# Kernel optimization log

Hardware: AMD Instinct MI355X
Metric: run time of the kernel (lower is better)

## Reference

```python
import jax, jax.numpy as jnp
import numpy as np

B, S, H, DFF, E, K = 2, 2048, 1024, 2048, 8, 2


def setup_inputs() -> dict:
    key = jax.random.key(0)
    ks = jax.random.split(key, 8)
    sc_h = 1.0 / np.sqrt(H)
    sc_f = 1.0 / np.sqrt(DFF)
    x = jax.random.normal(ks[0], (B, S, H), dtype=jnp.float32)
    Wg = jax.random.uniform(ks[1], (E, H), jnp.float32, -sc_h, sc_h)  # gate (no bias)
    W1 = jax.random.uniform(ks[2], (E, DFF, H), jnp.float32, -sc_h, sc_h)  # SiGLU gate proj
    b1 = jax.random.uniform(ks[3], (E, DFF), jnp.float32, -sc_h, sc_h)
    W2 = jax.random.uniform(ks[4], (E, DFF, H), jnp.float32, -sc_h, sc_h)  # SiGLU value proj
    b2 = jax.random.uniform(ks[5], (E, DFF), jnp.float32, -sc_h, sc_h)
    W3 = jax.random.uniform(ks[6], (E, H, DFF), jnp.float32, -sc_f, sc_f)  # down proj
    b3 = jax.random.uniform(ks[7], (E, H), jnp.float32, -sc_f, sc_f)
    return {"x": x, "Wg": Wg, "W1": W1, "b1": b1, "W2": W2, "b2": b2, "W3": W3, "b3": b3}


def _moe(x, Wg, W1, b1, W2, b2, W3, b3):
    Bm, Sm, Hm = x.shape
    xt = x.reshape(-1, Hm)  # [T, H]
    gout = xt @ Wg.T  # [T, E]
    topv, topi = jax.lax.top_k(gout, K)  # [T, K]
    w = jax.nn.softmax(topv, axis=-1)  # [T, K]
    # combine weights per expert: comb[t, e] = sum_k w[t,k] * 1[topi[t,k]==e]
    comb = jnp.einsum('tke,tk->te', jax.nn.one_hot(topi, E, dtype=x.dtype), w)  # [T, E]
    # dense per-expert FFN (fixed-shape equivalent of the gather/scatter loop)
    g = jnp.einsum('th,efh->etf', xt, W1) + b1[:, None, :]  # [E, T, DFF]
    v = jnp.einsum('th,efh->etf', xt, W2) + b2[:, None, :]
    h = jax.nn.silu(g) * v  # SiGLU
    eo = jnp.einsum('etf,ehf->eth', h, W3) + b3[:, None, :]  # [E, T, H]
    out = jnp.einsum('eth,te->th', eo, comb)
    return out.reshape(Bm, Sm, Hm)


def reference(x, Wg, W1, b1, W2, b2, W3, b3):
    return _moe(x, Wg, W1, b1, W2, b2, W3, b3)
```

## Files before the change

### kernel.cpp

```cpp
#include <hip/hip_runtime.h>
#include <hip/hip_bf16.h>

#define T_TOK 4096
#define H_DIM 1024
#define DFF_D 2048
#define E_NUM 8
#define K_TOP 2
#define MAXJOBS64 136
#define MAXJOBS128 72
#define CVT_BLOCKS 2048
#define EO_OFF ((size_t)T_TOK * K_TOP * H_DIM)

typedef __attribute__((ext_vector_type(8))) short s16x8;
typedef __attribute__((ext_vector_type(4))) float f32x4;

__device__ __forceinline__ ushort f2bf(float f) {
    unsigned u = __float_as_uint(f);
    u = (u + 0x7FFFu + ((u >> 16) & 1u)) >> 16;
    return (ushort)u;
}

__device__ __forceinline__ float bf2f(short s) {
    return __uint_as_float(((unsigned)(ushort)s) << 16);
}

__device__ __forceinline__ void glds16(const ushort* g, ushort* l) {
    __builtin_amdgcn_global_load_lds(
        (const __attribute__((address_space(1))) unsigned*)g,
        (__attribute__((address_space(3))) unsigned*)l, 16, 0, 0);
}

__device__ __forceinline__ s16x8 lds_frag(const ushort* base, int row, int bytecol) {
    int byte = row * 128 + (bytecol ^ ((row & 7) << 4));
    return *(const s16x8*)((const char*)base + byte);
}

__device__ __forceinline__ void cvt8(const float* p, ushort* dst, size_t i) {
    float4 a = ((const float4*)(p + i * 8))[0];
    float4 b = ((const float4*)(p + i * 8))[1];
    union { ushort us[8]; uint4 q; } o;
    o.us[0] = f2bf(a.x); o.us[1] = f2bf(a.y); o.us[2] = f2bf(a.z); o.us[3] = f2bf(a.w);
    o.us[4] = f2bf(b.x); o.us[5] = f2bf(b.y); o.us[6] = f2bf(b.z); o.us[7] = f2bf(b.w);
    ((uint4*)dst)[i] = o.q;
}

__global__ __launch_bounds__(256) void cvt_kernel(
    const float* __restrict__ in, ushort* __restrict__ out, int n8)
{
    int i = blockIdx.x * blockDim.x + threadIdx.x;
    const int stride = gridDim.x * blockDim.x;
    for (; i < n8; i += stride) cvt8(in, out, i);
}

__global__ __launch_bounds__(256) void cvtW_gate_kernel(
    const float* __restrict__ W1, ushort* __restrict__ w1bf,
    const float* __restrict__ W2, ushort* __restrict__ w2bf,
    const float* __restrict__ W3, ushort* __restrict__ w3bf,
    const float* __restrict__ x,  const float* __restrict__ Wg,
    int* __restrict__ topi_packed, float* __restrict__ wt_slot,
    ushort* __restrict__ xbf)
{
    if ((int)blockIdx.x < CVT_BLOCKS) {
        const int nW = E_NUM * DFF_D * H_DIM / 8;
        const int total = (W3 != nullptr) ? 3 * nW : 2 * nW;
        int i = blockIdx.x * 256 + threadIdx.x;
        const int stride = CVT_BLOCKS * 256;
        for (; i < total; i += stride) {
            if (i < nW)            cvt8(W1, w1bf, i);
            else if (i < 2 * nW)   cvt8(W2, w2bf, i - nW);
            else                   cvt8(W3, w3bf, i - 2 * nW);
        }
        return;
    }
    const int t = (blockIdx.x - CVT_BLOCKS) * 4 + (threadIdx.x >> 6);
    const int lane = threadIdx.x & 63;
    const float* xr = x + (size_t)t * H_DIM;
    float xv[16];
    #pragma unroll
    for (int j = 0; j < 16; ++j) xv[j] = xr[j * 64 + lane];

    ushort* xo = xbf + (size_t)t * H_DIM;
    #pragma unroll
    for (int j = 0; j < 16; ++j) xo[j * 64 + lane] = f2bf(xv[j]);

    float score[E_NUM];
    #pragma unroll
    for (int e = 0; e < E_NUM; ++e) {
        const float* wr = Wg + e * H_DIM;
        float p = 0.f;
        #pragma unroll
        for (int j = 0; j < 16; ++j) p += xv[j] * wr[j * 64 + lane];
        #pragma unroll
        for (int s = 32; s >= 1; s >>= 1) p += __shfl_xor(p, s, 64);
        score[e] = p;
    }
    if (lane == 0) {
        int i0 = 0;
        #pragma unroll
        for (int e = 1; e < E_NUM; ++e) if (score[e] > score[i0]) i0 = e;
        int i1 = (i0 == 0) ? 1 : 0;
        #pragma unroll
        for (int e = 0; e < E_NUM; ++e)
            if (e != i0 && score[e] > score[i1]) i1 = e;
        float e1 = expf(score[i1] - score[i0]);
        float w0 = 1.f / (1.f + e1);
        float w1 = e1 / (1.f + e1);
        topi_packed[t] = i0 | (i1 << 8);
        wt_slot[t * K_TOP + 0] = w0;
        wt_slot[t * K_TOP + 1] = w1;
    }
}

__global__ __launch_bounds__(256) void build_lists(
    const int* __restrict__ topi_packed,
    int* __restrict__ cnt, int* __restrict__ tok_list, int* __restrict__ slot_list)
{
    const int e = blockIdx.x;
    __shared__ int lcnt;
    if (threadIdx.x == 0) lcnt = 0;
    __syncthreads();
    for (int t = threadIdx.x; t < T_TOK; t += 256) {
        int pk = topi_packed[t];
        int i0 = pk & 0xff;
        int i1 = (pk >> 8) & 0xff;
        if (i0 == e) {
            int p = atomicAdd(&lcnt, 1);
            tok_list[e * T_TOK + p] = t;
            slot_list[e * T_TOK + p] = t * K_TOP + 0;
        }
        if (i1 == e) {
            int p = atomicAdd(&lcnt, 1);
            tok_list[e * T_TOK + p] = t;
            slot_list[e * T_TOK + p] = t * K_TOP + 1;
        }
    }
    __syncthreads();
    if (threadIdx.x == 0) cnt[e] = lcnt;
}

__global__ void build_jobs(const int* __restrict__ cnt,
                           int* __restrict__ jobs64, int* __restrict__ jobs128,
                           int* __restrict__ njobs)
{
    if (threadIdx.x == 0 && blockIdx.x == 0) {
        int n = 0, n2 = 0;
        for (int e = 0; e < E_NUM; ++e) {
            int mt = (cnt[e] + 63) >> 6;
            for (int m = 0; m < mt; ++m) jobs64[n++] = (e << 16) | m;
            int mt2 = (cnt[e] + 127) >> 7;
            for (int m = 0; m < mt2; ++m) jobs128[n2++] = (e << 16) | m;
        }
        njobs[0] = n;
        njobs[1] = n2;
    }
}

__global__ __launch_bounds__(256) void up_kernel(
    const ushort* __restrict__ xbf,
    const ushort* __restrict__ w1bf, const float* __restrict__ b1,
    const ushort* __restrict__ w2bf, const float* __restrict__ b2,
    const int* __restrict__ cnt, const int* __restrict__ tok_list,
    const int* __restrict__ slot_list, const float* __restrict__ wt_slot,
    const int* __restrict__ jobs128, const int* __restrict__ njobs,
    ushort* __restrict__ h)
{
    if ((int)blockIdx.y >= njobs[1]) return;
    const int jb = jobs128[blockIdx.y];
    const int e = jb >> 16;
    const int mbase = (jb & 0xffff) * 128;
    const int M = cnt[e];
    const int nbase = blockIdx.x * 64;
    const int tid = threadIdx.x;
    const int lane = tid & 63;
    const int w = tid >> 6;

    __shared__ ushort As[128 * 64];
    __shared__ ushort B1s[64 * 64];
    __shared__ ushort B2s[64 * 64];

    const ushort* srcA[4];
    const ushort* srcB1[2];
    const ushort* srcB2[2];
    #pragma unroll
    for (int j = 0; j < 4; ++j) {
        int o = j * 4096 + tid * 16;
        int r = o >> 7;
        int cb = (o & 127) ^ ((r & 7) << 4);
        int lpos = mbase + r; if (lpos > M - 1) lpos = M - 1;
        int tok = tok_list[e * T_TOK + lpos];
        srcA[j] = xbf + (size_t)tok * H_DIM + (cb >> 1);
    }
    #pragma unroll
    for (int j = 0; j < 2; ++j) {
        int o = j * 4096 + tid * 16;
        int r = o >> 7;
        int cb = (o & 127) ^ ((r & 7) << 4);
        srcB1[j] = w1bf + ((size_t)e * DFF_D + nbase + r) * H_DIM + (cb >> 1);
        srcB2[j] = w2bf + ((size_t)e * DFF_D + nbase + r) * H_DIM + (cb >> 1);
    }

    const f32x4 zero = {0.f, 0.f, 0.f, 0.f};
    f32x4 accg[2][4], accv[2][4];
    #pragma unroll
    for (int mi = 0; mi < 2; ++mi)
        #pragma unroll
        for (int ni = 0; ni < 4; ++ni) { accg[mi][ni] = zero; accv[mi][ni] = zero; }

    const int r16 = lane & 15;
    const int g4  = lane >> 4;
    const int cb0 = g4 * 16;

    for (int k0 = 0; k0 < H_DIM; k0 += 64) {
        #pragma unroll
        for (int j = 0; j < 4; ++j)
            glds16(srcA[j] + k0, &As[j * 2048 + tid * 8]);
        #pragma unroll
        for (int j = 0; j < 2; ++j) {
            glds16(srcB1[j] + k0, &B1s[j * 2048 + tid * 8]);
            glds16(srcB2[j] + k0, &B2s[j * 2048 + tid * 8]);
        }
        __syncthreads();
        #pragma unroll
        for (int kk = 0; kk < 2; ++kk) {
            s16x8 bf1[4], bf2[4];
            #pragma unroll
            for (int ni = 0; ni < 4; ++ni) {
                bf1[ni] = lds_frag(B1s, ni * 16 + r16, kk * 64 + cb0);
                bf2[ni] = lds_frag(B2s, ni * 16 + r16, kk * 64 + cb0);
            }
            #pragma unroll
            for (int mi = 0; mi < 2; ++mi) {
                s16x8 af = lds_frag(As, w * 32 + mi * 16 + r16, kk * 64 + cb0);
                #pragma unroll
                for (int ni = 0; ni < 4; ++ni) {
                    accg[mi][ni] = __builtin_amdgcn_mfma_f32_16x16x32_bf16(af, bf1[ni], accg[mi][ni], 0, 0, 0);
                    accv[mi][ni] = __builtin_amdgcn_mfma_f32_16x16x32_bf16(af, bf2[ni], accv[mi][ni], 0, 0, 0);
                }
            }
        }
        __syncthreads();
    }

    #pragma unroll
    for (int mi = 0; mi < 2; ++mi) {
        #pragma unroll
        for (int j = 0; j < 4; ++j) {
            int p = mbase + w * 32 + mi * 16 + g4 * 4 + j;
            if (p < M) {
                int slot = slot_list[e * T_TOK + p];
                float wgt = wt_slot[slot];
                #pragma unroll
                for (int ni = 0; ni < 4; ++ni) {
                    int col = nbase + ni * 16 + r16;
                    float g = accg[mi][ni][j] + b1[e * DFF_D + col];
                    float v = accv[mi][ni][j] + b2[e * DFF_D + col];
                    float s = g / (1.f + __expf(-g));
                    h[(size_t)slot * DFF_D + col] = f2bf(wgt * s * v);
                }
            }
        }
    }
}

__global__ __launch_bounds__(128) void down_kernel(
    const ushort* __restrict__ h,
    const ushort* __restrict__ w3bf,
    const int* __restrict__ cnt, const int* __restrict__ slot_list,
    const int* __restrict__ jobs128, const int* __restrict__ njobs,
    ushort* __restrict__ eo)
{
    if ((int)blockIdx.y >= njobs[1]) return;
    const int jb = jobs128[blockIdx.y];
    const int e = jb >> 16;
    const int mbase = (jb & 0xffff) * 128;
    const int M = cnt[e];
    const int nbase = (blockIdx.x >> 1) * 64;
    const int kc = blockIdx.x & 1;
    const int kbeg = kc * (DFF_D / 2);
    const int tid = threadIdx.x;
    const int lane = tid & 63;
    const int w = tid >> 6;

    __shared__ ushort As[128 * 64];
    __shared__ ushort Bs[64 * 64];

    const ushort* srcA[8];
    #pragma unroll
    for (int j = 0; j < 8; ++j) {
        int o = j * 2048 + tid * 16;
        int r = o >> 7;
        int cb = (o & 127) ^ ((r & 7) << 4);
        int lpos = mbase + r; if (lpos > M - 1) lpos = M - 1;
        int slot = slot_list[e * T_TOK + lpos];
        srcA[j] = h + (size_t)slot * DFF_D + kbeg + (cb >> 1);
    }
    const ushort* srcB[4];
    #pragma unroll
    for (int j = 0; j < 4; ++j) {
        int o = j * 2048 + tid * 16;
        int r = o >> 7;
        int cb = (o & 127) ^ ((r & 7) << 4);
        srcB[j] = w3bf + ((size_t)e * H_DIM + nbase + r) * DFF_D + kbeg + (cb >> 1);
    }

    const f32x4 zero = {0.f, 0.f, 0.f, 0.f};
    f32x4 acc[4][4];
    #pragma unroll
    for (int mi = 0; mi < 4; ++mi)
        #pragma unroll
        for (int ni = 0; ni < 4; ++ni) acc[mi][ni] = zero;

    const int r16 = lane & 15;
    const int g4  = lane >> 4;
    const int cb0 = g4 * 16;

    for (int k0 = 0; k0 < DFF_D / 2; k0 += 64) {
        #pragma unroll
        for (int j = 0; j < 8; ++j)
            glds16(srcA[j] + k0, &As[j * 1024 + tid * 8]);
        #pragma unroll
        for (int j = 0; j < 4; ++j)
            glds16(srcB[j] + k0, &Bs[j * 1024 + tid * 8]);
        __syncthreads();
        #pragma unroll
        for (int kk = 0; kk < 2; ++kk) {
            s16x8 bf[4];
            #pragma unroll
            for (int ni = 0; ni < 4; ++ni)
                bf[ni] = lds_frag(Bs, ni * 16 + r16, kk * 64 + cb0);
            #pragma unroll
            for (int mi = 0; mi < 4; ++mi) {
                s16x8 af = lds_frag(As, w * 64 + mi * 16 + r16, kk * 64 + cb0);
                #pragma unroll
                for (int ni = 0; ni < 4; ++ni)
                    acc[mi][ni] = __builtin_amdgcn_mfma_f32_16x16x32_bf16(af, bf[ni], acc[mi][ni], 0, 0, 0);
            }
        }
        __syncthreads();
    }

    ushort* eop = eo + (size_t)kc * EO_OFF;
    #pragma unroll
    for (int mi = 0; mi < 4; ++mi) {
        #pragma unroll
        for (int j = 0; j < 4; ++j) {
            int p = mbase + w * 64 + mi * 16 + g4 * 4 + j;
            if (p < M) {
                int slot = slot_list[e * T_TOK + p];
                #pragma unroll
                for (int ni = 0; ni < 4; ++ni) {
                    int col = nbase + ni * 16 + r16;
                    eop[(size_t)slot * H_DIM + col] = f2bf(acc[mi][ni][j]);
                }
            }
        }
    }
}

__global__ __launch_bounds__(256) void combine_kernel(
    const ushort* __restrict__ eo, const int* __restrict__ topi_packed,
    const float* __restrict__ wt_slot, const float* __restrict__ b3,
    float* __restrict__ out)
{
    const int i = blockIdx.x * 256 + threadIdx.x;
    const int t = i >> 7;
    const int c0 = (i & 127) * 8;
    const int pk = topi_packed[t];
    const int e0 = pk & 0xff, e1 = (pk >> 8) & 0xff;
    const float w0 = wt_slot[2 * t], w1 = wt_slot[2 * t + 1];
    s16x8 a0 = *(const s16x8*)(eo + (size_t)(2 * t) * H_DIM + c0);
    s16x8 b0 = *(const s16x8*)(eo + (size_t)(2 * t + 1) * H_DIM + c0);
    s16x8 a1 = *(const s16x8*)(eo + EO_OFF + (size_t)(2 * t) * H_DIM + c0);
    s16x8 b1 = *(const s16x8*)(eo + EO_OFF + (size_t)(2 * t + 1) * H_DIM + c0);
    const float4* p0 = (const float4*)(b3 + e0 * H_DIM + c0);
    const float4* p1 = (const float4*)(b3 + e1 * H_DIM + c0);
    float4 b0a = p0[0], b0b = p0[1];
    float4 b1a = p1[0], b1b = p1[1];
    float r[8];
    #pragma unroll
    for (int j = 0; j < 8; ++j)
        r[j] = (bf2f(a0[j]) + bf2f(a1[j])) + (bf2f(b0[j]) + bf2f(b1[j]));
    float4 r0, r1;
    r0.x = r[0] + w0 * b0a.x + w1 * b1a.x;
    r0.y = r[1] + w0 * b0a.y + w1 * b1a.y;
    r0.z = r[2] + w0 * b0a.z + w1 * b1a.z;
    r0.w = r[3] + w0 * b0a.w + w1 * b1a.w;
    r1.x = r[4] + w0 * b0b.x + w1 * b1b.x;
    r1.y = r[5] + w0 * b0b.y + w1 * b1b.y;
    r1.z = r[6] + w0 * b0b.z + w1 * b1b.z;
    r1.w = r[7] + w0 * b0b.w + w1 * b1b.w;
    float4* op = (float4*)(out + (size_t)t * H_DIM + c0);
    op[0] = r0;
    op[1] = r1;
}

extern "C" void kernel_launch(void* const* d_in, const int* in_sizes, int n_in,
                              void* d_out, int out_size, void* d_ws, size_t ws_size,
                              hipStream_t stream) {
    const float* x  = (const float*)d_in[0];
    const float* Wg = (const float*)d_in[1];
    const float* W1 = (const float*)d_in[2];
    const float* b1 = (const float*)d_in[3];
    const float* W2 = (const float*)d_in[4];
    const float* b2 = (const float*)d_in[5];
    const float* W3 = (const float*)d_in[6];
    const float* b3 = (const float*)d_in[7];
    float* out = (float*)d_out;

    char* ws = (char*)d_ws;
    int*   cnt       = (int*)(ws);
    int*   njobs     = (int*)(ws + 64);
    int*   jobs64    = (int*)(ws + 128);
    int*   jobs128   = (int*)(ws + 704);
    int*   tok_list  = (int*)(ws + 1024);
    int*   slot_list = (int*)(ws + 1024 + E_NUM * T_TOK * 4);
    float* wt_slot   = (float*)(ws + 1024 + 2 * E_NUM * T_TOK * 4);
    int*   topi      = (int*)(ws + 320 * 1024);
    ushort* xbf  = (ushort*)(ws + (size_t)1  * (1u << 20));
    ushort* w1bf = (ushort*)(ws + (size_t)16 * (1u << 20));
    ushort* w2bf = (ushort*)(ws + (size_t)48 * (1u << 20));
    ushort* hbuf = (ushort*)(ws + (size_t)80 * (1u << 20));
    ushort* eobf = (ushort*)(ws + (size_t)4  * (1u << 20));

    const bool bigws = ws_size >= ((size_t)147 << 20);
    ushort* w3bf = bigws ? (ushort*)(ws + (size_t)114 * (1u << 20))
                         : (ushort*)(ws + (size_t)40  * (1u << 20));

    cvtW_gate_kernel<<<CVT_BLOCKS + T_TOK / 4, 256, 0, stream>>>(
        W1, w1bf, W2, w2bf, bigws ? W3 : nullptr, w3bf,
        x, Wg, topi, wt_slot, xbf);

    build_lists<<<E_NUM, 256, 0, stream>>>(topi, cnt, tok_list, slot_list);
    build_jobs<<<1, 64, 0, stream>>>(cnt, jobs64, jobs128, njobs);

    dim3 gup(DFF_D / 64, MAXJOBS128);
    up_kernel<<<gup, 256, 0, stream>>>(xbf, w1bf, b1, w2bf, b2, cnt, tok_list,
                                       slot_list, wt_slot, jobs128, njobs, hbuf);

    if (!bigws)
        cvt_kernel<<<2048, 256, 0, stream>>>(W3, w3bf, E_NUM * H_DIM * DFF_D / 8);

    dim3 gdn((H_DIM / 64) * 2, MAXJOBS128);
    down_kernel<<<gdn, 128, 0, stream>>>(hbuf, w3bf, cnt, slot_list,
                                         jobs128, njobs, eobf);

    combine_kernel<<<T_TOK * H_DIM / 8 / 256, 256, 0, stream>>>(eobf, topi, wt_slot, b3, out);
}
```

Before: 257.2 us.

## Fold W3 conversion into up_kernel grid and derive jobs inline from counts

Removes the single-thread build_jobs launch; each GEMM block now derives its expert and row tile directly from cnt. In the big-workspace path, W3 fp32-to-bf16 conversion moves out of the first conversion kernel into extra block rows of up_kernel, so it overlaps with the up-projection GEMM instead of delaying gating. The eo buffers are split into two explicit pointers, which moves the second one to a new workspace offset. The risk is that the conversion blocks compete with the GEMM blocks for bandwidth and compute units.

```diff
diff --git a/kernel.cpp b/kernel.cpp
--- a/kernel.cpp
+++ b/kernel.cpp
@@ -6,10 +6,9 @@
 #define DFF_D 2048
 #define E_NUM 8
 #define K_TOP 2
-#define MAXJOBS64 136
 #define MAXJOBS128 72
 #define CVT_BLOCKS 2048
-#define EO_OFF ((size_t)T_TOK * K_TOP * H_DIM)
+#define W3_ROWS 8
 
 typedef __attribute__((ext_vector_type(8))) short s16x8;
 typedef __attribute__((ext_vector_type(4))) float f32x4;
@@ -44,6 +43,19 @@
     ((uint4*)dst)[i] = o.q;
 }
 
+__device__ __forceinline__ bool job_from_y(const int* cnt, int y, int& e, int& mbase, int& M) {
+    int n = 0; mbase = -1;
+    #pragma unroll
+    for (int ee = 0; ee < E_NUM; ++ee) {
+        int t = (cnt[ee] + 127) >> 7;
+        if (mbase < 0 && y < n + t) { e = ee; mbase = (y - n) * 128; }
+        n += t;
+    }
+    if (mbase < 0) return false;
+    M = cnt[e];
+    return true;
+}
+
 __global__ __launch_bounds__(256) void cvt_kernel(
     const float* __restrict__ in, ushort* __restrict__ out, int n8)
 {
@@ -55,20 +67,17 @@
 __global__ __launch_bounds__(256) void cvtW_gate_kernel(
     const float* __restrict__ W1, ushort* __restrict__ w1bf,
     const float* __restrict__ W2, ushort* __restrict__ w2bf,
-    const float* __restrict__ W3, ushort* __restrict__ w3bf,
     const float* __restrict__ x,  const float* __restrict__ Wg,
     int* __restrict__ topi_packed, float* __restrict__ wt_slot,
     ushort* __restrict__ xbf)
 {
     if ((int)blockIdx.x < CVT_BLOCKS) {
         const int nW = E_NUM * DFF_D * H_DIM / 8;
-        const int total = (W3 != nullptr) ? 3 * nW : 2 * nW;
         int i = blockIdx.x * 256 + threadIdx.x;
         const int stride = CVT_BLOCKS * 256;
-        for (; i < total; i += stride) {
-            if (i < nW)            cvt8(W1, w1bf, i);
-            else if (i < 2 * nW)   cvt8(W2, w2bf, i - nW);
-            else                   cvt8(W3, w3bf, i - 2 * nW);
+        for (; i < 2 * nW; i += stride) {
+            if (i < nW) cvt8(W1, w1bf, i);
+            else        cvt8(W2, w2bf, i - nW);
         }
         return;
     }
@@ -138,37 +147,26 @@
     if (threadIdx.x == 0) cnt[e] = lcnt;
 }
 
-__global__ void build_jobs(const int* __restrict__ cnt,
-                           int* __restrict__ jobs64, int* __restrict__ jobs128,
-                           int* __restrict__ njobs)
-{
-    if (threadIdx.x == 0 && blockIdx.x == 0) {
-        int n = 0, n2 = 0;
-        for (int e = 0; e < E_NUM; ++e) {
-            int mt = (cnt[e] + 63) >> 6;
-            for (int m = 0; m < mt; ++m) jobs64[n++] = (e << 16) | m;
-            int mt2 = (cnt[e] + 127) >> 7;
-            for (int m = 0; m < mt2; ++m) jobs128[n2++] = (e << 16) | m;
-        }
-        njobs[0] = n;
-        njobs[1] = n2;
-    }
-}
-
 __global__ __launch_bounds__(256) void up_kernel(
     const ushort* __restrict__ xbf,
     const ushort* __restrict__ w1bf, const float* __restrict__ b1,
     const ushort* __restrict__ w2bf, const float* __restrict__ b2,
     const int* __restrict__ cnt, const int* __restrict__ tok_list,
     const int* __restrict__ slot_list, const float* __restrict__ wt_slot,
-    const int* __restrict__ jobs128, const int* __restrict__ njobs,
+    const float* __restrict__ W3src, ushort* __restrict__ w3dst,
     ushort* __restrict__ h)
 {
-    if ((int)blockIdx.y >= njobs[1]) return;
-    const int jb = jobs128[blockIdx.y];
-    const int e = jb >> 16;
-    const int mbase = (jb & 0xffff) * 128;
-    const int M = cnt[e];
+    if ((int)blockIdx.y >= MAXJOBS128) {
+        if (W3src != nullptr) {
+            const int nW3 = E_NUM * H_DIM * DFF_D / 8;
+            int i = ((blockIdx.y - MAXJOBS128) * gridDim.x + blockIdx.x) * 256 + threadIdx.x;
+            const int stride = W3_ROWS * gridDim.x * 256;
+            for (; i < nW3; i += stride) cvt8(W3src, w3dst, i);
+        }
+        return;
+    }
+    int e, mbase, M;
+    if (!job_from_y(cnt, blockIdx.y, e, mbase, M)) return;
     const int nbase = blockIdx.x * 64;
     const int tid = threadIdx.x;
     const int lane = tid & 63;
@@ -266,14 +264,10 @@
     const ushort* __restrict__ h,
     const ushort* __restrict__ w3bf,
     const int* __restrict__ cnt, const int* __restrict__ slot_list,
-    const int* __restrict__ jobs128, const int* __restrict__ njobs,
-    ushort* __restrict__ eo)
-{
-    if ((int)blockIdx.y >= njobs[1]) return;
-    const int jb = jobs128[blockIdx.y];
-    const int e = jb >> 16;
-    const int mbase = (jb & 0xffff) * 128;
-    const int M = cnt[e];
+    ushort* __restrict__ eo0, ushort* __restrict__ eo1)
+{
+    int e, mbase, M;
+    if (!job_from_y(cnt, blockIdx.y, e, mbase, M)) return;
     const int nbase = (blockIdx.x >> 1) * 64;
     const int kc = blockIdx.x & 1;
     const int kbeg = kc * (DFF_D / 2);
@@ -339,7 +333,7 @@
         __syncthreads();
     }
 
-    ushort* eop = eo + (size_t)kc * EO_OFF;
+    ushort* eop = kc ? eo1 : eo0;
     #pragma unroll
     for (int mi = 0; mi < 4; ++mi) {
         #pragma unroll
@@ -358,7 +352,8 @@
 }
 
 __global__ __launch_bounds__(256) void combine_kernel(
-    const ushort* __restrict__ eo, const int* __restrict__ topi_packed,
+    const ushort* __restrict__ eo0, const ushort* __restrict__ eo1,
+    const int* __restrict__ topi_packed,
     const float* __restrict__ wt_slot, const float* __restrict__ b3,
     float* __restrict__ out)
 {
@@ -368,10 +363,10 @@
     const int pk = topi_packed[t];
     const int e0 = pk & 0xff, e1 = (pk >> 8) & 0xff;
     const float w0 = wt_slot[2 * t], w1 = wt_slot[2 * t + 1];
-    s16x8 a0 = *(const s16x8*)(eo + (size_t)(2 * t) * H_DIM + c0);
-    s16x8 b0 = *(const s16x8*)(eo + (size_t)(2 * t + 1) * H_DIM + c0);
-    s16x8 a1 = *(const s16x8*)(eo + EO_OFF + (size_t)(2 * t) * H_DIM + c0);
-    s16x8 b1 = *(const s16x8*)(eo + EO_OFF + (size_t)(2 * t + 1) * H_DIM + c0);
+    s16x8 a0 = *(const s16x8*)(eo0 + (size_t)(2 * t) * H_DIM + c0);
+    s16x8 b0 = *(const s16x8*)(eo0 + (size_t)(2 * t + 1) * H_DIM + c0);
+    s16x8 a1 = *(const s16x8*)(eo1 + (size_t)(2 * t) * H_DIM + c0);
+    s16x8 b1 = *(const s16x8*)(eo1 + (size_t)(2 * t + 1) * H_DIM + c0);
     const float4* p0 = (const float4*)(b3 + e0 * H_DIM + c0);
     const float4* p1 = (const float4*)(b3 + e1 * H_DIM + c0);
     float4 b0a = p0[0], b0b = p0[1];
@@ -409,9 +404,6 @@
 
     char* ws = (char*)d_ws;
     int*   cnt       = (int*)(ws);
-    int*   njobs     = (int*)(ws + 64);
-    int*   jobs64    = (int*)(ws + 128);
-    int*   jobs128   = (int*)(ws + 704);
     int*   tok_list  = (int*)(ws + 1024);
     int*   slot_list = (int*)(ws + 1024 + E_NUM * T_TOK * 4);
     float* wt_slot   = (float*)(ws + 1024 + 2 * E_NUM * T_TOK * 4);
@@ -420,29 +412,28 @@
     ushort* w1bf = (ushort*)(ws + (size_t)16 * (1u << 20));
     ushort* w2bf = (ushort*)(ws + (size_t)48 * (1u << 20));
     ushort* hbuf = (ushort*)(ws + (size_t)80 * (1u << 20));
-    ushort* eobf = (ushort*)(ws + (size_t)4  * (1u << 20));
+    ushort* eo0 = (ushort*)(ws + (size_t)4  * (1u << 20));
+    ushort* eo1 = (ushort*)(ws + (size_t)21 * (1u << 20));
 
     const bool bigws = ws_size >= ((size_t)147 << 20);
     ushort* w3bf = bigws ? (ushort*)(ws + (size_t)114 * (1u << 20))
                          : (ushort*)(ws + (size_t)40  * (1u << 20));
 
     cvtW_gate_kernel<<<CVT_BLOCKS + T_TOK / 4, 256, 0, stream>>>(
-        W1, w1bf, W2, w2bf, bigws ? W3 : nullptr, w3bf,
-        x, Wg, topi, wt_slot, xbf);
+        W1, w1bf, W2, w2bf, x, Wg, topi, wt_slot, xbf);
 
     build_lists<<<E_NUM, 256, 0, stream>>>(topi, cnt, tok_list, slot_list);
-    build_jobs<<<1, 64, 0, stream>>>(cnt, jobs64, jobs128, njobs);
-
-    dim3 gup(DFF_D / 64, MAXJOBS128);
+
+    dim3 gup(DFF_D / 64, MAXJOBS128 + W3_ROWS);
     up_kernel<<<gup, 256, 0, stream>>>(xbf, w1bf, b1, w2bf, b2, cnt, tok_list,
-                                       slot_list, wt_slot, jobs128, njobs, hbuf);
+                                       slot_list, wt_slot,
+                                       bigws ? W3 : nullptr, w3bf, hbuf);
 
     if (!bigws)
         cvt_kernel<<<2048, 256, 0, stream>>>(W3, w3bf, E_NUM * H_DIM * DFF_D / 8);
 
     dim3 gdn((H_DIM / 64) * 2, MAXJOBS128);
-    down_kernel<<<gdn, 128, 0, stream>>>(hbuf, w3bf, cnt, slot_list,
-                                         jobs128, njobs, eobf);
-
-    combine_kernel<<<T_TOK * H_DIM / 8 / 256, 256, 0, stream>>>(eobf, topi, wt_slot, b3, out);
-}
+    down_kernel<<<gdn, 128, 0, stream>>>(hbuf, w3bf, cnt, slot_list, eo0, eo1);
+
+    combine_kernel<<<T_TOK * H_DIM / 8 / 256, 256, 0, stream>>>(eo0, eo1, topi, wt_slot, b3, out);
+}
```

After: 247.8 us. 1.04x faster.
